# Optimization experiments

Measured on AMD Instinct MI355X. Metric: run time of the kernel, lower is better.

The kernel has to match this reference:

```python
import jax, jax.numpy as jnp
import numpy as np

DIM = 256
NUM_HEADS = 8
HEAD_DIM = DIM // NUM_HEADS  # 32
SCALE = HEAD_DIM ** (-0.5)


def _conv1x1(x, w, b):
    # x: [B,C,H,W], w: [O,C,1,1], b: [O]
    return jnp.einsum('bchw,oc->bohw', x, w[:, :, 0, 0]) + b[None, :, None, None]


def _dwconv3x3(x, w, b):
    # depthwise conv, groups=C, padding=1 (SAME)
    y = jax.lax.conv_general_dilated(
        x, w, window_strides=(1, 1), padding='SAME',
        feature_group_count=x.shape[1],
        dimension_numbers=('NCHW', 'OIHW', 'NCHW'))
    return y + b[None, :, None, None]


def setup_inputs() -> dict:
    key = jax.random.key(0)
    ks = jax.random.split(key, 9)
    s = 0.05
    return {
        'x': jax.random.normal(ks[0], (4, DIM, 48, 48), jnp.float32),
        'w_qk': jax.random.normal(ks[1], (2 * DIM, DIM, 1, 1), jnp.float32) * s,
        'b_qk': jax.random.normal(ks[2], (2 * DIM,), jnp.float32) * s,
        'w_v': jax.random.normal(ks[3], (DIM, DIM, 1, 1), jnp.float32) * s,
        'b_v': jax.random.normal(ks[4], (DIM,), jnp.float32) * s,
        'w_pe': jax.random.normal(ks[5], (DIM, 1, 3, 3), jnp.float32) * s,
        'b_pe': jax.random.normal(ks[6], (DIM,), jnp.float32) * s,
        'w_proj': jax.random.normal(ks[7], (DIM, DIM, 1, 1), jnp.float32) * s,
        'b_proj': jax.random.normal(ks[8], (DIM,), jnp.float32) * s,
    }


def reference(x, w_qk, b_qk, w_v, b_v, w_pe, b_pe, w_proj, b_proj):
    B, C, H, W = x.shape
    N = H * W
    h, d = NUM_HEADS, HEAD_DIM

    qk = _conv1x1(x, w_qk, b_qk).reshape(B, h, 2 * d, N)
    v4 = _conv1x1(x, w_v, b_v)                # [B,C,H,W]
    pe = _dwconv3x3(v4, w_pe, b_pe)           # [B,C,H,W]
    v = v4.reshape(B, h, d, N)

    q, k = qk[:, :, :d, :], qk[:, :, d:, :]   # [B,h,d,N] each
    attn = jnp.einsum('bhdi,bhdj->bhij', q, k) * SCALE  # [B,h,N,N]
    attn = jax.nn.softmax(attn, axis=-1)
    out = jnp.einsum('bhdj,bhij->bhdi', v, attn)        # [B,h,d,N]
    out = out.reshape(B, C, H, W)

    return _conv1x1(out + pe, w_proj, b_proj)
```

## Files before the change

### kernel.cpp

```cpp
#include <hip/hip_runtime.h>
#include <hip/hip_bf16.h>

#define NPIX 2304
#define HW 48
#define CDIM 256
#define NHEADS 8
#define HD 32
#define SCALE_CONST 0.17677669529663687f
#define LOG2E 1.4426950408889634f

typedef __attribute__((ext_vector_type(8))) short  short8v;
typedef __attribute__((ext_vector_type(4))) short  short4v;
typedef __attribute__((ext_vector_type(4))) float  floatx4;

__device__ inline short f2bf(float f) {
    unsigned u = __builtin_bit_cast(unsigned, f);
    u += 0x7FFFu + ((u >> 16) & 1u);
    return (short)(u >> 16);
}
__device__ inline float bf2f(unsigned short us) {
    return __builtin_bit_cast(float, (unsigned)us << 16);
}
__device__ inline float fexp2(float x) {
    return __builtin_amdgcn_exp2f(x);
}

__global__ __launch_bounds__(256) void prep_kernel(
    const float* __restrict__ x,
    short* __restrict__ XT,
    const float* __restrict__ wqk, const float* __restrict__ wv,
    const float* __restrict__ wp,
    short* __restrict__ wqkb, short* __restrict__ wvb, short* __restrict__ wpb)
{
    const int bx = blockIdx.x;
    const int t = threadIdx.x;
    if (bx >= 576) {
        int tid = (bx - 576) * 256 + t;
        for (int idx = tid; idx < 262144; idx += 16384) {
            if (idx < 131072)       wqkb[idx] = f2bf(wqk[idx]);
            else if (idx < 196608)  wvb[idx - 131072] = f2bf(wv[idx - 131072]);
            else                    wpb[idx - 196608] = f2bf(wp[idx - 196608]);
        }
        return;
    }
    __shared__ float sT[64][65];
    const int nt = bx % 36, ct = (bx / 36) & 3, b = bx / 144;
    const int c0 = ct * 64, n0 = nt * 64;
    const float* sp = x + ((size_t)b * 256 + c0) * NPIX + n0;
    const int cl = t >> 6, n = t & 63;
#pragma unroll
    for (int it = 0; it < 16; ++it) {
        int c = it * 4 + cl;
        sT[n][c] = sp[(size_t)c * NPIX + n];
    }
    __syncthreads();
    const int nr = t >> 2, q = t & 3;
    short out[16];
#pragma unroll
    for (int j = 0; j < 16; ++j) out[j] = f2bf(sT[nr][q * 16 + j]);
    short* dp = XT + ((size_t)b * NPIX + n0 + nr) * 256 + c0 + q * 16;
    *(int4*)dp = *(int4*)out;
    *(int4*)(dp + 8) = *(int4*)(out + 8);
}

#define XROW 528

__device__ inline void stage_xt_tile(const short* __restrict__ src_base,
                                     char* __restrict__ sX, int t)
{
    const short* src = src_base + (size_t)(t >> 3) * 256 + (t & 7) * 32;
    char* dst = sX + (t >> 3) * XROW + (t & 7) * 64;
#pragma unroll
    for (int rr = 0; rr < 2; ++rr) {
        const short* s = src + rr * 32 * 256;
        char* d = dst + rr * 32 * XROW;
        *(int4*)d        = *(const int4*)s;
        *(int4*)(d + 16) = *(const int4*)(s + 8);
        *(int4*)(d + 32) = *(const int4*)(s + 16);
        *(int4*)(d + 48) = *(const int4*)(s + 24);
    }
}

__global__ __launch_bounds__(256) void conv_qkv_mfma(
    const short* __restrict__ Wqk,
    const short* __restrict__ Wv,
    const float* __restrict__ bqk,
    const float* __restrict__ bv,
    const short* __restrict__ XT,
    short* __restrict__ QT,
    short* __restrict__ KT,
    short* __restrict__ VB)
{
    __shared__ __align__(16) char sX[64 * XROW];
    const int n0 = blockIdx.x * 64;
    const int b  = blockIdx.z;
    const int t = threadIdx.x, lane = t & 63, w = t >> 6;
    const int l15 = lane & 15, quad = lane >> 4;

    stage_xt_tile(XT + ((size_t)b * NPIX + n0) * 256, sX, t);
    __syncthreads();

    floatx4 accs[2][4];
#pragma unroll
    for (int g = 0; g < 2; ++g) {
        const int og = blockIdx.y + g * 6;
        const bool isV = (og >= 8);
        const short* Wb = isV ? Wv + (size_t)((og - 8) * 64 + w * 16 + l15) * CDIM
                              : Wqk + (size_t)(og * 64 + w * 16 + l15) * CDIM;
#pragma unroll
        for (int ib = 0; ib < 4; ++ib) accs[g][ib] = (floatx4){0.f, 0.f, 0.f, 0.f};
#pragma unroll
        for (int s = 0; s < 8; ++s) {
            short8v af = *(const short8v*)(Wb + s * 32 + quad * 8);
#pragma unroll
            for (int ib = 0; ib < 4; ++ib) {
                short8v bf = *(const short8v*)(sX + (ib * 16 + l15) * XROW + s * 64 + quad * 16);
                accs[g][ib] = __builtin_amdgcn_mfma_f32_16x16x32_bf16(af, bf, accs[g][ib], 0, 0, 0);
            }
        }
    }

#pragma unroll
    for (int g = 0; g < 2; ++g) {
        const int og = blockIdx.y + g * 6;
        const bool isV = (og >= 8);
        __syncthreads();
        if (!isV) {
            const bool isQ = (w < 2);
            const float scl = isQ ? SCALE_CONST * LOG2E : 1.0f;
            float bvv[4];
#pragma unroll
            for (int r = 0; r < 4; ++r) bvv[r] = bqk[og * 64 + w * 16 + quad * 4 + r];
#pragma unroll
            for (int ib = 0; ib < 4; ++ib) {
                short pb[4];
#pragma unroll
                for (int r = 0; r < 4; ++r) pb[r] = f2bf((accs[g][ib][r] + bvv[r]) * scl);
                *(short4v*)(sX + (ib * 16 + l15) * 136 + (w * 16 + quad * 4) * 2) = *(short4v*)pb;
            }
            __syncthreads();
            const int n = t >> 2, q = t & 3;
            int4 v0 = *(const int4*)(sX + n * 136 + q * 32);
            int4 v1 = *(const int4*)(sX + n * 136 + q * 32 + 16);
            short* dst = ((q < 2) ? QT : KT)
                       + ((size_t)(b * 8 + og) * NPIX + n0 + n) * HD + (q & 1) * 16;
            *(int4*)dst = v0;
            *(int4*)(dst + 8) = v1;
        } else {
            const int o0 = (og - 8) * 64 + w * 16 + quad * 4;
            float bvv[4];
#pragma unroll
            for (int r = 0; r < 4; ++r) bvv[r] = bv[o0 + r];
#pragma unroll
            for (int ib = 0; ib < 4; ++ib) {
                short pb[4];
#pragma unroll
                for (int r = 0; r < 4; ++r) pb[r] = f2bf(accs[g][ib][r] + bvv[r]);
                *(short4v*)(sX + (ib * 16 + l15) * 132 + (w * 16 + quad * 4) * 2) = *(short4v*)pb;
            }
            __syncthreads();
            const int o = t >> 2, q = t & 3;
            short tmp[16];
#pragma unroll
            for (int k = 0; k < 16; ++k)
                tmp[k] = *(const short*)(sX + (q * 16 + k) * 132 + o * 2);
            short* dst = VB + ((size_t)b * 256 + (og - 8) * 64 + o) * NPIX + n0 + q * 16;
            *(int4*)dst = *(int4*)tmp;
            *(int4*)(dst + 8) = *(int4*)(tmp + 8);
        }
    }
}

#define KROW 72
#define VROW 136
#define PROW 136
#define SK0 0
#define SK1 4608
#define SV0 9216
#define SV1 13568
#define SP0 17920
#define FL_SMEM 26624
#define DROW 170

__global__ __launch_bounds__(256) void flash_attn_mfma(
    const short* __restrict__ QT,
    const short* __restrict__ KT,
    const short* __restrict__ VB,
    const float* __restrict__ w_pe,
    const float* __restrict__ b_pe,
    short* __restrict__ ST)
{
    __shared__ __align__(16) char smem[FL_SMEM];

    const int i0 = blockIdx.x * 64;
    const int bh = blockIdx.y;
    const int b  = bh >> 3, hh = bh & 7;

    const short* KTp = KT + (size_t)bh * NPIX * HD;
    const short* Vp  = VB + (size_t)(b * 256 + hh * HD) * NPIX;

    const int t    = threadIdx.x;
    const int lane = t & 63;
    const int w    = t >> 6;
    const int l15  = lane & 15;
    const int quad = lane >> 4;

    const short8v qfrag = *(const short8v*)(
        QT + ((size_t)bh * NPIX + i0 + w * 16 + l15) * HD + quad * 8);

    short8v ones;
#pragma unroll
    for (int k = 0; k < 8; ++k) ones[k] = (short)0x3F80;

    char* const sPw = smem + SP0 + w * (16 * PROW);

    floatx4 oacc[2], lacc;
    oacc[0] = (floatx4){0.f, 0.f, 0.f, 0.f};
    oacc[1] = (floatx4){0.f, 0.f, 0.f, 0.f};
    lacc    = (floatx4){0.f, 0.f, 0.f, 0.f};

    const short* ksrc = KTp + (size_t)(t >> 2) * HD + (t & 3) * 8;
    const short* vsrc = Vp + (size_t)(t >> 3) * NPIX + (t & 7) * 8;
    const int koff = (t >> 2) * KROW + (t & 3) * 16;
    const int voff = (t >> 3) * VROW + (t & 7) * 16;

    int4 kst = *(const int4*)ksrc;
    int4 vst = *(const int4*)vsrc;

    for (int it = 0; it < 36; ++it) {
        char* bufK = smem + ((it & 1) ? SK1 : SK0);
        char* bufV = smem + ((it & 1) ? SV1 : SV0);
        *(int2*)(bufK + koff)     = *(int2*)&kst;
        *(int2*)(bufK + koff + 8) = *((int2*)&kst + 1);
        *(int2*)(bufV + voff)     = *(int2*)&vst;
        *(int2*)(bufV + voff + 8) = *((int2*)&vst + 1);
        if (it + 1 < 36) {
            kst = *(const int4*)(ksrc + (size_t)(it + 1) * 64 * HD);
            vst = *(const int4*)(vsrc + (it + 1) * 64);
        }
        __syncthreads();

        floatx4 sacc[4];
#pragma unroll
        for (int jb = 0; jb < 4; ++jb) {
            const char* ka = bufK + (jb * 16 + l15) * KROW + quad * 16;
            short8v af;
            ((int2*)&af)[0] = *(const int2*)ka;
            ((int2*)&af)[1] = *(const int2*)(ka + 8);
            sacc[jb] = __builtin_amdgcn_mfma_f32_16x16x32_bf16(
                af, qfrag, (floatx4){0.f, 0.f, 0.f, 0.f}, 0, 0, 0);
        }

#pragma unroll
        for (int jb = 0; jb < 4; ++jb) {
            unsigned tb[4];
#pragma unroll
            for (int r = 0; r < 4; ++r)
                tb[r] = __builtin_bit_cast(unsigned, fexp2(sacc[jb][r]));
            int2 pw;
            pw.x = (int)__builtin_amdgcn_perm(tb[1], tb[0], 0x07060302u);
            pw.y = (int)__builtin_amdgcn_perm(tb[3], tb[2], 0x07060302u);
            *(int2*)(sPw + l15 * PROW + jb * 32 + quad * 8) = pw;
        }

#pragma unroll
        for (int ks = 0; ks < 2; ++ks) {
            const char* pa = sPw + l15 * PROW + ks * 64 + quad * 16;
            short8v pf;
            ((int2*)&pf)[0] = *(const int2*)pa;
            ((int2*)&pf)[1] = *(const int2*)(pa + 8);
#pragma unroll
            for (int db = 0; db < 2; ++db) {
                const char* va = bufV + (db * 16 + l15) * VROW + ks * 64 + quad * 16;
                short8v vf;
                ((int2*)&vf)[0] = *(const int2*)va;
                ((int2*)&vf)[1] = *(const int2*)(va + 8);
                oacc[db] = __builtin_amdgcn_mfma_f32_16x16x32_bf16(vf, pf, oacc[db], 0, 0, 0);
            }
            lacc = __builtin_amdgcn_mfma_f32_16x16x32_bf16(ones, pf, lacc, 0, 0, 0);
        }
    }

    const float invl = 1.0f / lacc[0];
    __syncthreads();

    short* const sO    = (short*)smem;
    short* const sHalo = (short*)(smem + 4608);

    {
        const int il = w * 16 + l15;
#pragma unroll
        for (int db = 0; db < 2; ++db) {
            short ob[4];
#pragma unroll
            for (int r = 0; r < 4; ++r) ob[r] = f2bf(oacc[db][r] * invl);
            *(short4v*)(sO + il * 36 + db * 16 + quad * 4) = *(short4v*)ob;
        }
    }
    for (int ch8 = t; ch8 < 672; ch8 += 256) {
        int ch = ch8 / 21, off = (ch8 % 21) * 8;
        int base = i0 - 52 + off;
        const short* src = VB + ((size_t)b * 256 + hh * HD + ch) * NPIX;
        short tmp[8];
        if (base >= 0 && base + 8 <= NPIX) {
            *(int4*)tmp = *(const int4*)(src + base);
        } else {
#pragma unroll
            for (int u = 0; u < 8; ++u) {
                int p = base + u;
                tmp[u] = (p >= 0 && p < NPIX) ? src[p] : (short)0;
            }
        }
        *(int4*)&sHalo[ch * DROW + off] = *(int4*)tmp;
    }
    __syncthreads();

    {
        const int d  = t & 31;
        const int pg = t >> 5;
        const int c  = hh * HD + d;
        float wv[9];
#pragma unroll
        for (int k = 0; k < 9; ++k) wv[k] = w_pe[c * 9 + k];
        const float bb = b_pe[c];
        const int px0  = i0 + pg * 8;
        const int col0 = px0 % HW;
        const short* sprow = &sHalo[d * DROW + 52 + pg * 8];
        short* stp = ST + ((size_t)b * NPIX + px0) * 256 + c;

#pragma unroll
        for (int u = 0; u < 8; ++u) {
            int colu = col0 + u; if (colu >= HW) colu -= HW;
            const bool okL = (colu != 0), okR = (colu != HW - 1);
            float a = bb;
#pragma unroll
            for (int dy = 0; dy < 3; ++dy) {
                int ci = u + (dy - 1) * HW;
                a += wv[dy * 3 + 1] * bf2f((unsigned short)sprow[ci]);
                if (okL) a += wv[dy * 3 + 0] * bf2f((unsigned short)sprow[ci - 1]);
                if (okR) a += wv[dy * 3 + 2] * bf2f((unsigned short)sprow[ci + 1]);
            }
            float o = bf2f((unsigned short)sO[(pg * 8 + u) * 36 + d]);
            stp[(size_t)u * 256] = f2bf(o + a);
        }
    }
}

__global__ __launch_bounds__(256) void conv_proj_mfma(
    const short* __restrict__ Wb,
    const float* __restrict__ bias,
    const short* __restrict__ ST,
    float* __restrict__ out)
{
    __shared__ __align__(16) char sX[64 * XROW];
    const int n0 = blockIdx.x * 64;
    const int og = blockIdx.y;
    const int b  = blockIdx.z;
    const int t = threadIdx.x, lane = t & 63, w = t >> 6;
    const int l15 = lane & 15, quad = lane >> 4;

    stage_xt_tile(ST + ((size_t)b * NPIX + n0) * 256, sX, t);
    __syncthreads();

    const short* Arow = Wb + (size_t)(og * 64 + w * 16 + l15) * CDIM;
    floatx4 acc[4];
#pragma unroll
    for (int ib = 0; ib < 4; ++ib) acc[ib] = (floatx4){0.f, 0.f, 0.f, 0.f};
#pragma unroll
    for (int s = 0; s < 8; ++s) {
        short8v af = *(const short8v*)(Arow + s * 32 + quad * 8);
#pragma unroll
        for (int ib = 0; ib < 4; ++ib) {
            short8v bf = *(const short8v*)(sX + (ib * 16 + l15) * XROW + s * 64 + quad * 16);
            acc[ib] = __builtin_amdgcn_mfma_f32_16x16x32_bf16(af, bf, acc[ib], 0, 0, 0);
        }
    }
    __syncthreads();

    {
        float bvv[4];
#pragma unroll
        for (int r = 0; r < 4; ++r) bvv[r] = bias[og * 64 + w * 16 + quad * 4 + r];
        float* sRep = (float*)sX;
#pragma unroll
        for (int r = 0; r < 4; ++r)
#pragma unroll
            for (int ib = 0; ib < 4; ++ib)
                sRep[(w * 16 + quad * 4 + r) * 68 + ib * 16 + l15] = acc[ib][r] + bvv[r];
    }
    __syncthreads();

    const int o = t >> 2, q = t & 3;
    const float* src = (const float*)sX + o * 68 + q * 16;
    float* dst = out + ((size_t)b * 256 + og * 64 + o) * NPIX + n0 + q * 16;
#pragma unroll
    for (int k = 0; k < 4; ++k)
        *(int4*)(dst + k * 4) = *(const int4*)(src + k * 4);
}

extern "C" void kernel_launch(void* const* d_in, const int* in_sizes, int n_in,
                              void* d_out, int out_size, void* d_ws, size_t ws_size,
                              hipStream_t stream) {
    const float* x      = (const float*)d_in[0];
    const float* w_qk   = (const float*)d_in[1];
    const float* b_qk   = (const float*)d_in[2];
    const float* w_v    = (const float*)d_in[3];
    const float* b_v    = (const float*)d_in[4];
    const float* w_pe   = (const float*)d_in[5];
    const float* b_pe   = (const float*)d_in[6];
    const float* w_proj = (const float*)d_in[7];
    const float* b_proj = (const float*)d_in[8];
    float* out = (float*)d_out;

    char* wsb = (char*)d_ws;
    short* ws_xt  = (short*)wsb;  wsb += (size_t)4 * NPIX * 256 * 2;
    short* ws_qt  = (short*)wsb;  wsb += (size_t)32 * NPIX * HD * 2;
    short* ws_kt  = (short*)wsb;  wsb += (size_t)32 * NPIX * HD * 2;
    short* ws_vb  = (short*)wsb;  wsb += (size_t)4 * 256 * NPIX * 2;
    short* ws_st  = (short*)wsb;  wsb += (size_t)4 * NPIX * 256 * 2;
    short* ws_wqk = (short*)wsb;  wsb += (size_t)512 * 256 * 2;
    short* ws_wv  = (short*)wsb;  wsb += (size_t)256 * 256 * 2;
    short* ws_wp  = (short*)wsb;  wsb += (size_t)256 * 256 * 2;

    prep_kernel<<<dim3(640), 256, 0, stream>>>(x, ws_xt, w_qk, w_v, w_proj,
                                               ws_wqk, ws_wv, ws_wp);
    conv_qkv_mfma<<<dim3(36, 6, 4), 256, 0, stream>>>(ws_wqk, ws_wv, b_qk, b_v,
                                                      ws_xt, ws_qt, ws_kt, ws_vb);
    flash_attn_mfma<<<dim3(36, 32), 256, 0, stream>>>(ws_qt, ws_kt, ws_vb,
                                                      w_pe, b_pe, ws_st);
    conv_proj_mfma<<<dim3(36, 4, 4), 256, 0, stream>>>(ws_wp, b_proj, ws_st, out);
}
```

Baseline: 159.4 us.

## Fuse input transpose and weight bf16 conversion into conv kernels, drop prep kernel

Removes the separate prep kernel that transposed x to bf16 and converted all weights to bf16. conv_qkv now loads fp32 x directly, converts it and transposes it into shared memory, and both conv kernels convert their fp32 weight fragments to bf16 on the fly. This saves one kernel launch and the global write and re-read of the transposed activations. In exchange, each block converts weights redundantly and reads twice as many bytes for weights, and the shared-memory stores are scattered 2-byte writes that may cause bank conflicts.

```diff
diff --git a/kernel.cpp b/kernel.cpp
--- a/kernel.cpp
+++ b/kernel.cpp
@@ -25,45 +25,16 @@
     return __builtin_amdgcn_exp2f(x);
 }
 
-__global__ __launch_bounds__(256) void prep_kernel(
-    const float* __restrict__ x,
-    short* __restrict__ XT,
-    const float* __restrict__ wqk, const float* __restrict__ wv,
-    const float* __restrict__ wp,
-    short* __restrict__ wqkb, short* __restrict__ wvb, short* __restrict__ wpb)
-{
-    const int bx = blockIdx.x;
-    const int t = threadIdx.x;
-    if (bx >= 576) {
-        int tid = (bx - 576) * 256 + t;
-        for (int idx = tid; idx < 262144; idx += 16384) {
-            if (idx < 131072)       wqkb[idx] = f2bf(wqk[idx]);
-            else if (idx < 196608)  wvb[idx - 131072] = f2bf(wv[idx - 131072]);
-            else                    wpb[idx - 196608] = f2bf(wp[idx - 196608]);
-        }
-        return;
-    }
-    __shared__ float sT[64][65];
-    const int nt = bx % 36, ct = (bx / 36) & 3, b = bx / 144;
-    const int c0 = ct * 64, n0 = nt * 64;
-    const float* sp = x + ((size_t)b * 256 + c0) * NPIX + n0;
-    const int cl = t >> 6, n = t & 63;
-#pragma unroll
-    for (int it = 0; it < 16; ++it) {
-        int c = it * 4 + cl;
-        sT[n][c] = sp[(size_t)c * NPIX + n];
-    }
-    __syncthreads();
-    const int nr = t >> 2, q = t & 3;
-    short out[16];
-#pragma unroll
-    for (int j = 0; j < 16; ++j) out[j] = f2bf(sT[nr][q * 16 + j]);
-    short* dp = XT + ((size_t)b * NPIX + n0 + nr) * 256 + c0 + q * 16;
-    *(int4*)dp = *(int4*)out;
-    *(int4*)(dp + 8) = *(int4*)(out + 8);
-}
-
 #define XROW 528
+
+__device__ inline short8v wfrag_f32(const float* __restrict__ p) {
+    floatx4 a0 = *(const floatx4*)p;
+    floatx4 a1 = *(const floatx4*)(p + 4);
+    short8v r;
+#pragma unroll
+    for (int k = 0; k < 4; ++k) { r[k] = f2bf(a0[k]); r[k + 4] = f2bf(a1[k]); }
+    return r;
+}
 
 __device__ inline void stage_xt_tile(const short* __restrict__ src_base,
                                      char* __restrict__ sX, int t)
@@ -82,11 +53,11 @@
 }
 
 __global__ __launch_bounds__(256) void conv_qkv_mfma(
-    const short* __restrict__ Wqk,
-    const short* __restrict__ Wv,
+    const float* __restrict__ x,
+    const float* __restrict__ Wqk,
+    const float* __restrict__ Wv,
     const float* __restrict__ bqk,
     const float* __restrict__ bv,
-    const short* __restrict__ XT,
     short* __restrict__ QT,
     short* __restrict__ KT,
     short* __restrict__ VB)
@@ -97,7 +68,18 @@
     const int t = threadIdx.x, lane = t & 63, w = t >> 6;
     const int l15 = lane & 15, quad = lane >> 4;
 
-    stage_xt_tile(XT + ((size_t)b * NPIX + n0) * 256, sX, t);
+    {
+        const int ps = t & 15;
+        const int cb = t >> 4;
+#pragma unroll
+        for (int pass = 0; pass < 16; ++pass) {
+            int c = pass * 16 + cb;
+            floatx4 f = *(const floatx4*)(x + ((size_t)b * 256 + c) * NPIX + n0 + ps * 4);
+#pragma unroll
+            for (int k = 0; k < 4; ++k)
+                *(short*)(sX + (ps * 4 + k) * XROW + c * 2) = f2bf(f[k]);
+        }
+    }
     __syncthreads();
 
     floatx4 accs[2][4];
@@ -105,13 +87,13 @@
     for (int g = 0; g < 2; ++g) {
         const int og = blockIdx.y + g * 6;
         const bool isV = (og >= 8);
-        const short* Wb = isV ? Wv + (size_t)((og - 8) * 64 + w * 16 + l15) * CDIM
-                              : Wqk + (size_t)(og * 64 + w * 16 + l15) * CDIM;
+        const float* Wrow = (isV ? Wv + (size_t)((og - 8) * 64 + w * 16 + l15) * CDIM
+                                 : Wqk + (size_t)(og * 64 + w * 16 + l15) * CDIM) + quad * 8;
 #pragma unroll
         for (int ib = 0; ib < 4; ++ib) accs[g][ib] = (floatx4){0.f, 0.f, 0.f, 0.f};
 #pragma unroll
         for (int s = 0; s < 8; ++s) {
-            short8v af = *(const short8v*)(Wb + s * 32 + quad * 8);
+            short8v af = wfrag_f32(Wrow + s * 32);
 #pragma unroll
             for (int ib = 0; ib < 4; ++ib) {
                 short8v bf = *(const short8v*)(sX + (ib * 16 + l15) * XROW + s * 64 + quad * 16);
@@ -347,7 +329,7 @@
 }
 
 __global__ __launch_bounds__(256) void conv_proj_mfma(
-    const short* __restrict__ Wb,
+    const float* __restrict__ Wp,
     const float* __restrict__ bias,
     const short* __restrict__ ST,
     float* __restrict__ out)
@@ -362,13 +344,13 @@
     stage_xt_tile(ST + ((size_t)b * NPIX + n0) * 256, sX, t);
     __syncthreads();
 
-    const short* Arow = Wb + (size_t)(og * 64 + w * 16 + l15) * CDIM;
+    const float* Arow = Wp + (size_t)(og * 64 + w * 16 + l15) * CDIM + quad * 8;
     floatx4 acc[4];
 #pragma unroll
     for (int ib = 0; ib < 4; ++ib) acc[ib] = (floatx4){0.f, 0.f, 0.f, 0.f};
 #pragma unroll
     for (int s = 0; s < 8; ++s) {
-        short8v af = *(const short8v*)(Arow + s * 32 + quad * 8);
+        short8v af = wfrag_f32(Arow + s * 32);
 #pragma unroll
         for (int ib = 0; ib < 4; ++ib) {
             short8v bf = *(const short8v*)(sX + (ib * 16 + l15) * XROW + s * 64 + quad * 16);
@@ -413,20 +395,14 @@
     float* out = (float*)d_out;
 
     char* wsb = (char*)d_ws;
-    short* ws_xt  = (short*)wsb;  wsb += (size_t)4 * NPIX * 256 * 2;
     short* ws_qt  = (short*)wsb;  wsb += (size_t)32 * NPIX * HD * 2;
     short* ws_kt  = (short*)wsb;  wsb += (size_t)32 * NPIX * HD * 2;
     short* ws_vb  = (short*)wsb;  wsb += (size_t)4 * 256 * NPIX * 2;
     short* ws_st  = (short*)wsb;  wsb += (size_t)4 * NPIX * 256 * 2;
-    short* ws_wqk = (short*)wsb;  wsb += (size_t)512 * 256 * 2;
-    short* ws_wv  = (short*)wsb;  wsb += (size_t)256 * 256 * 2;
-    short* ws_wp  = (short*)wsb;  wsb += (size_t)256 * 256 * 2;
-
-    prep_kernel<<<dim3(640), 256, 0, stream>>>(x, ws_xt, w_qk, w_v, w_proj,
-                                               ws_wqk, ws_wv, ws_wp);
-    conv_qkv_mfma<<<dim3(36, 6, 4), 256, 0, stream>>>(ws_wqk, ws_wv, b_qk, b_v,
-                                                      ws_xt, ws_qt, ws_kt, ws_vb);
+
+    conv_qkv_mfma<<<dim3(36, 6, 4), 256, 0, stream>>>(x, w_qk, w_v, b_qk, b_v,
+                                                      ws_qt, ws_kt, ws_vb);
     flash_attn_mfma<<<dim3(36, 32), 256, 0, stream>>>(ws_qt, ws_kt, ws_vb,
                                                       w_pe, b_pe, ws_st);
-    conv_proj_mfma<<<dim3(36, 4, 4), 256, 0, stream>>>(ws_wp, b_proj, ws_st, out);
-}
+    conv_proj_mfma<<<dim3(36, 4, 4), 256, 0, stream>>>(w_proj, b_proj, ws_st, out);
+}
```

After: 163.6 us. 1.03x slower.
